# Kernel optimization log

Hardware: AMD Instinct MI355X
Metric: run time of the kernel (lower is better)

The kernel has to match this reference:

```python
import jax, jax.numpy as jnp
import numpy as np

B, T, D, H = 2, 2048, 1024, 16
HS = D // H  # head_size = 64
DFF = 4 * D


def setup_inputs() -> dict:
    key = jax.random.key(0)
    ks = jax.random.split(key, 12)
    s = 0.02
    return {
        "x": jax.random.normal(ks[0], (B, T, D), dtype=jnp.float32),
        "Wq": jax.random.normal(ks[1], (D, D), dtype=jnp.float32) * s,
        "Wk": jax.random.normal(ks[2], (D, D), dtype=jnp.float32) * s,
        "Wv": jax.random.normal(ks[3], (D, D), dtype=jnp.float32) * s,
        "Wo": jax.random.normal(ks[4], (D, D), dtype=jnp.float32) * s,
        "bo": jnp.zeros((D,), dtype=jnp.float32),
        "W1": jax.random.normal(ks[5], (D, DFF), dtype=jnp.float32) * s,
        "b1": jnp.zeros((DFF,), dtype=jnp.float32),
        "W2": jax.random.normal(ks[6], (DFF, D), dtype=jnp.float32) * s,
        "b2": jnp.zeros((D,), dtype=jnp.float32),
        "g1": jnp.ones((D,), dtype=jnp.float32),
        "be1": jnp.zeros((D,), dtype=jnp.float32),
        "g2": jnp.ones((D,), dtype=jnp.float32),
        "be2": jnp.zeros((D,), dtype=jnp.float32),
    }


def layer_norm(x, g, b, eps=1e-5):
    mu = jnp.mean(x, axis=-1, keepdims=True)
    var = jnp.var(x, axis=-1, keepdims=True)
    return (x - mu) * jax.lax.rsqrt(var + eps) * g + b


def attention(x, Wq, Wk, Wv, Wo, bo):
    # x: [B,T,D] -> q,k,v: [B,H,T,HS]
    def split_heads(y):
        return y.reshape(B, T, H, HS).transpose(0, 2, 1, 3)
    q = split_heads(x @ Wq)
    k = split_heads(x @ Wk)
    v = split_heads(x @ Wv)
    scores = jnp.einsum("bhqd,bhkd->bhqk", q, k) / jnp.sqrt(jnp.float32(HS))
    causal = jnp.tril(jnp.ones((T, T), dtype=bool))
    scores = jnp.where(causal, scores, -jnp.inf)
    probs = jax.nn.softmax(scores, axis=-1)
    out = jnp.einsum("bhqk,bhkd->bhqd", probs, v)
    out = out.transpose(0, 2, 1, 3).reshape(B, T, D)
    return out @ Wo + bo


def reference(x, Wq, Wk, Wv, Wo, bo, W1, b1, W2, b2, g1, be1, g2, be2):
    x = x + attention(layer_norm(x, g1, be1), Wq, Wk, Wv, Wo, bo)
    h = layer_norm(x, g2, be2)
    x = x + (jax.nn.relu(h @ W1 + b1) @ W2 + b2)
    return x
```

## Files before the change

### kernel.cpp

```cpp
#include <hip/hip_runtime.h>
#include <stdint.h>

#define Bc   2
#define Tc   2048
#define Dc   1024
#define Hc   16
#define HSc  64
#define DFFc 4096
#define Mc   (Bc * Tc)

using f32x4 = __attribute__((ext_vector_type(4))) float;
using s16x8 = __attribute__((ext_vector_type(8))) short;

__device__ __forceinline__ ushort f2bf(float f) {
  union { float f; uint32_t u; } v; v.f = f;
  uint32_t r = (v.u + 0x7FFFu + ((v.u >> 16) & 1u)) >> 16;
  return (ushort)r;
}
__device__ __forceinline__ float bf2f(ushort u) {
  union { uint32_t u; float f; } v; v.u = ((uint32_t)u) << 16;
  return v.f;
}
__device__ __forceinline__ uint32_t cvtpk(float a, float b) {
  uint32_t r;
  asm volatile("v_cvt_pk_bf16_f32 %0, %1, %2" : "=v"(r) : "v"(a), "v"(b));
  return r;
}
__device__ __forceinline__ float wredsum(float v) {
#pragma unroll
  for (int o = 32; o > 0; o >>= 1) v += __shfl_down(v, o);
  return v;
}

__device__ __forceinline__ void gload16(const ushort* g, ushort* l) {
  __builtin_amdgcn_global_load_lds(
      (const __attribute__((address_space(1))) void*)g,
      (__attribute__((address_space(3))) void*)l, 16, 0, 0);
}

__global__ __launch_bounds__(256) void tcast_all_kernel(
    const float* __restrict__ Wq, const float* __restrict__ Wk,
    const float* __restrict__ Wv, const float* __restrict__ Wo,
    const float* __restrict__ W1, const float* __restrict__ W2,
    ushort* __restrict__ wqkvt, ushort* __restrict__ wot,
    ushort* __restrict__ w1t, ushort* __restrict__ w2t) {
  __shared__ float t[32][33];
  const int id = blockIdx.x;
  const float* src; ushort* dst; int K, N, bx, by;
  if (id < 4096) {
    const int which = id >> 10, local = id & 1023;
    src = (which == 0) ? Wq : (which == 1) ? Wk : (which == 2) ? Wv : Wo;
    dst = (which == 3) ? wot : wqkvt + (size_t)which * 1024 * 1024;
    K = 1024; N = 1024; bx = local & 31; by = local >> 5;
  } else if (id < 8192) {
    const int local = id - 4096;
    src = W1; dst = w1t; K = 1024; N = 4096;
    bx = local & 127; by = local >> 7;
  } else {
    const int local = id - 8192;
    src = W2; dst = w2t; K = 4096; N = 1024;
    bx = local & 31; by = local >> 5;
  }
  const int tid = threadIdx.x;
  const int n0 = bx * 32, k0 = by * 32;
  const int r = tid >> 3, c4 = (tid & 7) * 4;
  const float4 v = *(const float4*)&src[(size_t)(k0 + r) * N + n0 + c4];
  t[r][c4] = v.x; t[r][c4 + 1] = v.y; t[r][c4 + 2] = v.z; t[r][c4 + 3] = v.w;
  __syncthreads();
  ushort4 o;
  o.x = f2bf(t[c4 + 0][r]); o.y = f2bf(t[c4 + 1][r]);
  o.z = f2bf(t[c4 + 2][r]); o.w = f2bf(t[c4 + 3][r]);
  *(ushort4*)&dst[(size_t)(n0 + r) * K + k0 + c4] = o;
}

__global__ __launch_bounds__(256) void ln_kernel(const float* __restrict__ x,
                                                 const float* __restrict__ g,
                                                 const float* __restrict__ b,
                                                 ushort* __restrict__ out) {
  const int row = blockIdx.x;
  const int tid = threadIdx.x;
  const int lane = tid & 63, wave = tid >> 6;
  const float4 v = ((const float4*)(x + (size_t)row * Dc))[tid];
  float s  = v.x + v.y + v.z + v.w;
  float s2 = v.x * v.x + v.y * v.y + v.z * v.z + v.w * v.w;
  __shared__ float rs[4], rs2[4];
  s = wredsum(s); s2 = wredsum(s2);
  if (lane == 0) { rs[wave] = s; rs2[wave] = s2; }
  __syncthreads();
  const float S  = rs[0] + rs[1] + rs[2] + rs[3];
  const float S2 = rs2[0] + rs2[1] + rs2[2] + rs2[3];
  const float mu = S * (1.f / (float)Dc);
  const float rstd = rsqrtf(S2 * (1.f / (float)Dc) - mu * mu + 1e-5f);
  const float4 gv = ((const float4*)g)[tid];
  const float4 bv = ((const float4*)b)[tid];
  ushort4 o;
  o.x = f2bf((v.x - mu) * rstd * gv.x + bv.x);
  o.y = f2bf((v.y - mu) * rstd * gv.y + bv.y);
  o.z = f2bf((v.z - mu) * rstd * gv.z + bv.z);
  o.w = f2bf((v.w - mu) * rstd * gv.w + bv.w);
  ((ushort4*)(out + (size_t)row * Dc))[tid] = o;
}

template <int BM, int NSPLIT, int OUT_BF16, int RELU, int BIAS, int RES, int QKVSPLIT>
__global__ __launch_bounds__(256) void gemm3_kernel(
    const ushort* __restrict__ A, const ushort* __restrict__ Bt,
    const float* __restrict__ bias, const float* __restrict__ res,
    void* __restrict__ C0, void* __restrict__ C1, void* __restrict__ C2,
    int M, int N, int K) {
  constexpr int MF = BM / 32;
  __shared__ __align__(16) ushort As[BM * 64];
  __shared__ __align__(16) ushort Bs[128 * 64];
  const int tid = threadIdx.x;
  const int lane = tid & 63, w = tid >> 6;
  const int wm = w >> 1, wn = w & 1;
  const int row0 = blockIdx.x * BM, col0 = blockIdx.y * 128;
  const int fr = lane & 15, fg = lane >> 4;
  const int kbeg = (NSPLIT > 1) ? blockIdx.z * (K / NSPLIT) : 0;
  const int kend = (NSPLIT > 1) ? kbeg + K / NSPLIT : K;

  f32x4 acc[MF][4] = {};

  for (int k0 = kbeg; k0 < kend; k0 += 64) {
#pragma unroll
    for (int i = 0; i < BM * 8 / 256; i++) {
      const int c = i * 256 + tid;
      const int r = c >> 3, j = c & 7;
      gload16(A + (size_t)(row0 + r) * K + k0 + ((j ^ (r & 7)) << 3),
              As + (i * 256 + w * 64) * 8);
    }
#pragma unroll
    for (int i = 0; i < 4; i++) {
      const int c = i * 256 + tid;
      const int r = c >> 3, j = c & 7;
      gload16(Bt + (size_t)(col0 + r) * K + k0 + ((j ^ (r & 7)) << 3),
              Bs + (i * 256 + w * 64) * 8);
    }
    __syncthreads();

#pragma unroll
    for (int kk = 0; kk < 2; kk++) {
      const int js = ((kk * 4 + fg) ^ (fr & 7)) << 3;
      s16x8 af[MF], bfr[4];
#pragma unroll
      for (int m = 0; m < MF; m++)
        af[m] = *(const s16x8*)&As[(wm * (BM / 2) + m * 16 + fr) * 64 + js];
#pragma unroll
      for (int n = 0; n < 4; n++)
        bfr[n] = *(const s16x8*)&Bs[(wn * 64 + n * 16 + fr) * 64 + js];
#pragma unroll
      for (int m = 0; m < MF; m++)
#pragma unroll
        for (int n = 0; n < 4; n++)
          acc[m][n] = __builtin_amdgcn_mfma_f32_16x16x32_bf16(af[m], bfr[n], acc[m][n], 0, 0, 0);
    }
    __syncthreads();
  }

  if (NSPLIT > 1) {
    float* P = (float*)C0 + (size_t)blockIdx.z * M * N;
#pragma unroll
    for (int m = 0; m < MF; m++)
#pragma unroll
      for (int n = 0; n < 4; n++)
#pragma unroll
        for (int i = 0; i < 4; i++) {
          const int r = row0 + wm * (BM / 2) + m * 16 + fg * 4 + i;
          const int c = col0 + n * 16 + wn * 64 + fr;
          P[(size_t)r * N + c] = acc[m][n][i];
        }
    return;
  }

  void* Cb = C0;
  int cbase = col0;
  if (QKVSPLIT) {
    const int which = col0 >> 10;
    Cb = (which == 0) ? C0 : (which == 1) ? C1 : C2;
    cbase = col0 & 1023;
  }
  const int NW = QKVSPLIT ? 1024 : N;
#pragma unroll
  for (int m = 0; m < MF; m++) {
#pragma unroll
    for (int n = 0; n < 4; n++) {
#pragma unroll
      for (int i = 0; i < 4; i++) {
        const int r = row0 + wm * (BM / 2) + m * 16 + fg * 4 + i;
        const int c = cbase + wn * 64 + n * 16 + fr;
        float v = acc[m][n][i];
        if (BIAS) v += bias[col0 - cbase + c];
        if (RELU) v = fmaxf(v, 0.f);
        if (RES)  v += res[(size_t)r * NW + c];
        if (OUT_BF16) ((ushort*)Cb)[(size_t)r * NW + c] = f2bf(v);
        else          ((float*)Cb)[(size_t)r * NW + c] = v;
      }
    }
  }
}

__global__ __launch_bounds__(256) void sum2_kernel(const float* __restrict__ p0,
                                                   const float* __restrict__ p1,
                                                   const float* __restrict__ bias,
                                                   const float* __restrict__ res,
                                                   float* __restrict__ out) {
  const size_t i = ((size_t)blockIdx.x * 256 + threadIdx.x) * 4;
  const float4 a = *(const float4*)(p0 + i);
  const float4 b = *(const float4*)(p1 + i);
  const float4 r = *(const float4*)(res + i);
  const float4 bs = *(const float4*)(bias + (i & 1023));
  float4 o;
  o.x = a.x + b.x + bs.x + r.x;
  o.y = a.y + b.y + bs.y + r.y;
  o.z = a.z + b.z + bs.z + r.z;
  o.w = a.w + b.w + bs.w + r.w;
  *(float4*)(out + i) = o;
}

__global__ __launch_bounds__(512) void fattn3_kernel(const ushort* __restrict__ Q,
                                                     const ushort* __restrict__ K,
                                                     const ushort* __restrict__ V,
                                                     float* __restrict__ pacc,
                                                     float* __restrict__ pl) {
  __shared__ __align__(16) ushort Kl[2][64][72];
  __shared__ __align__(16) ushort Vt[2][64][72];
  __shared__ __align__(16) uint32_t Pu[8][512];

  const int tid = threadIdx.x;
  const int lane = tid & 63, w = tid >> 6;
  const int fr = lane & 15, fg = lane >> 4;

  const int bh   = blockIdx.x & 31;
  const int rest = blockIdx.x >> 5;
  const int qb   = 15 - (rest >> 1);
  const int z    = rest & 1;
  const int h = bh & 15, b = bh >> 4;
  const int q0 = qb * 128;
  const size_t hbase = (size_t)b * Tc * Dc + (size_t)h * HSc;

  s16x8 qf0, qf1;
  {
    const ushort* qp = Q + hbase + (size_t)(q0 + w * 16 + fr) * Dc + fg * 8;
    qf0 = *(const s16x8*)(qp);
    qf1 = *(const s16x8*)(qp + 32);
  }

  const int kkey = tid >> 3, kd8 = (tid & 7) * 8;
  const int vkey = tid & 63, vd8 = (tid >> 6) * 8;

  const int t0 = z * (qb + 1), t1 = (z + 1) * (qb + 1);
  uint4 kreg = *(const uint4*)(K + hbase + (size_t)(t0 * 64 + kkey) * Dc + kd8);
  uint4 vreg = *(const uint4*)(V + hbase + (size_t)(t0 * 64 + vkey) * Dc + vd8);

  f32x4 acc[4] = {};
  float ps = 0.f;
  const float Cs = 0.18033688f;

  for (int kt = t0; kt < t1; kt++) {
    const int cur = (kt - t0) & 1;
    *(uint4*)&Kl[cur][kkey][kd8] = kreg;
    {
      union { uint4 v; ushort u[8]; } t; t.v = vreg;
#pragma unroll
      for (int j = 0; j < 8; j++) Vt[cur][vd8 + j][vkey] = t.u[j];
    }
    if (kt + 1 < t1) {
      kreg = *(const uint4*)(K + hbase + (size_t)((kt + 1) * 64 + kkey) * Dc + kd8);
      vreg = *(const uint4*)(V + hbase + (size_t)((kt + 1) * 64 + vkey) * Dc + vd8);
    }
    __syncthreads();

    const bool skip = (kt * 64 > q0 + w * 16 + 15);
    if (!skip) {
      f32x4 s[4] = {};
      __builtin_amdgcn_s_setprio(1);
#pragma unroll
      for (int kf = 0; kf < 4; kf++) {
        const s16x8 k0 = *(const s16x8*)&Kl[cur][kf * 16 + fr][fg * 8];
        const s16x8 k1 = *(const s16x8*)&Kl[cur][kf * 16 + fr][32 + fg * 8];
        s[kf] = __builtin_amdgcn_mfma_f32_16x16x32_bf16(k0, qf0, s[kf], 0, 0, 0);
        s[kf] = __builtin_amdgcn_mfma_f32_16x16x32_bf16(k1, qf1, s[kf], 0, 0, 0);
      }
      __builtin_amdgcn_s_setprio(0);

      const bool diag = (kt * 64 + 63 > q0 + w * 16);
      const int qg = q0 + w * 16 + fr;
#pragma unroll
      for (int kf = 0; kf < 4; kf++) {
        float p[4];
#pragma unroll
        for (int i = 0; i < 4; i++) {
          p[i] = exp2f(s[kf][i] * Cs);
          if (diag) {
            const int kg = kt * 64 + kf * 16 + fg * 4 + i;
            if (kg > qg) p[i] = 0.f;
          }
          ps += p[i];
        }
        uint2 pk;
        pk.x = cvtpk(p[0], p[1]);
        pk.y = cvtpk(p[2], p[3]);
        *(uint2*)&Pu[w][(2 * kf + (fg >> 1)) * 64 + fr * 4 + (fg & 1) * 2] = pk;
      }

      const s16x8 pa0 = *(const s16x8*)&Pu[w][fg * 64 + fr * 4];
      const s16x8 pa1 = *(const s16x8*)&Pu[w][(4 + fg) * 64 + fr * 4];
      __builtin_amdgcn_s_setprio(1);
#pragma unroll
      for (int df = 0; df < 4; df++) {
        const s16x8 v0 = *(const s16x8*)&Vt[cur][df * 16 + fr][fg * 8];
        const s16x8 v1 = *(const s16x8*)&Vt[cur][df * 16 + fr][32 + fg * 8];
        acc[df] = __builtin_amdgcn_mfma_f32_16x16x32_bf16(pa0, v0, acc[df], 0, 0, 0);
        acc[df] = __builtin_amdgcn_mfma_f32_16x16x32_bf16(pa1, v1, acc[df], 0, 0, 0);
      }
      __builtin_amdgcn_s_setprio(0);
    }
  }

  ps += __shfl_xor(ps, 16);
  ps += __shfl_xor(ps, 32);
  if (lane < 16)
    pl[(size_t)z * (32 * 2048) + (size_t)bh * 2048 + q0 + w * 16 + lane] = ps;

  float* pa = pacc + (size_t)z * (32ull * 2048 * 64) + (size_t)bh * 2048 * 64;
#pragma unroll
  for (int i = 0; i < 4; i++) {
    const int qr = q0 + w * 16 + fg * 4 + i;
#pragma unroll
    for (int df = 0; df < 4; df++)
      pa[(size_t)qr * 64 + df * 16 + fr] = acc[df][i];
  }
}

__global__ __launch_bounds__(256) void amerge_kernel(const float* __restrict__ pacc,
                                                     const float* __restrict__ pl,
                                                     ushort* __restrict__ O) {
  const int g = blockIdx.x * 256 + threadIdx.x;
  const int d4 = g & 15;
  const int t  = (g >> 4) & 2047;
  const int bh = g >> 15;
  const int h = bh & 15, b = bh >> 4;
  const size_t base = ((size_t)bh * 2048 + t) * 64 + d4 * 4;
  const float4 a = *(const float4*)(pacc + base);
  const float4 c = *(const float4*)(pacc + 32ull * 2048 * 64 + base);
  const float inv = 1.f / (pl[(size_t)bh * 2048 + t] + pl[32 * 2048 + (size_t)bh * 2048 + t]);
  ushort4 o;
  o.x = f2bf((a.x + c.x) * inv);
  o.y = f2bf((a.y + c.y) * inv);
  o.z = f2bf((a.z + c.z) * inv);
  o.w = f2bf((a.w + c.w) * inv);
  *(ushort4*)&O[((size_t)(b * 2048 + t)) * 1024 + h * 64 + d4 * 4] = o;
}

extern "C" void kernel_launch(void* const* d_in, const int* in_sizes, int n_in,
                              void* d_out, int out_size, void* d_ws, size_t ws_size,
                              hipStream_t stream) {
  const float* x   = (const float*)d_in[0];
  const float* Wq  = (const float*)d_in[1];
  const float* Wk  = (const float*)d_in[2];
  const float* Wv  = (const float*)d_in[3];
  const float* Wo  = (const float*)d_in[4];
  const float* bo  = (const float*)d_in[5];
  const float* W1  = (const float*)d_in[6];
  const float* b1  = (const float*)d_in[7];
  const float* W2  = (const float*)d_in[8];
  const float* b2  = (const float*)d_in[9];
  const float* g1  = (const float*)d_in[10];
  const float* be1 = (const float*)d_in[11];
  const float* g2  = (const float*)d_in[12];
  const float* be2 = (const float*)d_in[13];

  char* ws = (char*)d_ws;
  const size_t MB = 1ull << 20;
  ushort* ln1   = (ushort*)(ws + 0 * MB);
  ushort* qb    = (ushort*)(ws + 8 * MB);
  ushort* kb    = (ushort*)(ws + 16 * MB);
  ushort* vb    = (ushort*)(ws + 24 * MB);
  ushort* wqkvt = (ushort*)(ws + 32 * MB);
  ushort* wot   = (ushort*)(ws + 38 * MB);
  ushort* w1t   = (ushort*)(ws + 40 * MB);
  ushort* w2t   = (ushort*)(ws + 48 * MB);
  float*  x1    = (float*)(ws + 56 * MB);
  ushort* hb    = (ushort*)(ws + 72 * MB);
  float*  pacc  = (float*)(ws + 56 * MB);
  float*  plv   = (float*)(ws + 88 * MB);
  float*  fpart = (float*)(ws + 0 * MB);

  tcast_all_kernel<<<12288, 256, 0, stream>>>(Wq, Wk, Wv, Wo, W1, W2,
                                              wqkvt, wot, w1t, w2t);

  ln_kernel<<<Mc, 256, 0, stream>>>(x, g1, be1, ln1);

  gemm3_kernel<128, 1, 1, 0, 0, 0, 1><<<dim3(32, 24), 256, 0, stream>>>(
      ln1, wqkvt, nullptr, nullptr, qb, kb, vb, Mc, 3072, Dc);

  fattn3_kernel<<<1024, 512, 0, stream>>>(qb, kb, vb, pacc, plv);
  amerge_kernel<<<4096, 256, 0, stream>>>(pacc, plv, ln1);

  gemm3_kernel<64, 1, 0, 0, 1, 1, 0><<<dim3(64, 8), 256, 0, stream>>>(
      ln1, wot, bo, x, x1, nullptr, nullptr, Mc, Dc, Dc);

  ln_kernel<<<Mc, 256, 0, stream>>>(x1, g2, be2, qb);

  gemm3_kernel<128, 1, 1, 1, 1, 0, 0><<<dim3(32, 32), 256, 0, stream>>>(
      qb, w1t, b1, nullptr, hb, nullptr, nullptr, Mc, DFFc, Dc);

  gemm3_kernel<64, 2, 0, 0, 0, 0, 0><<<dim3(64, 8, 2), 256, 0, stream>>>(
      hb, w2t, nullptr, nullptr, fpart, nullptr, nullptr, Mc, Dc, DFFc);
  sum2_kernel<<<4096, 256, 0, stream>>>(fpart, fpart + (size_t)Mc * Dc, b2, x1,
                                        (float*)d_out);
}
```

Measured before the change: 222.4 us.

## Add 8-wave GEMM with 256-wide tiles and double-buffered direct-to-LDS loads

Introduces gemm8_kernel, which runs 512 threads per block with larger output tiles (256 columns, 128-256 rows). It double-buffers global-to-LDS loads with explicit vmcnt waits and uses 16x16x32 bf16 MFMA with an XOR-swizzled LDS layout. It replaces gemm3 for the QKV, FFN1 and FFN2 projections to raise data reuse per tile and overlap loads with compute. The trade-off is fewer blocks per GEMM (for example 192 for QKV), which can leave compute units idle, plus higher LDS and register pressure.

```diff
diff --git a/kernel.cpp b/kernel.cpp
--- a/kernel.cpp
+++ b/kernel.cpp
@@ -36,6 +36,12 @@
   __builtin_amdgcn_global_load_lds(
       (const __attribute__((address_space(1))) void*)g,
       (__attribute__((address_space(3))) void*)l, 16, 0, 0);
+}
+
+template <int N> __device__ __forceinline__ void vwait() {
+  if constexpr (N == 0) asm volatile("s_waitcnt vmcnt(0)" ::: "memory");
+  else if constexpr (N == 6) asm volatile("s_waitcnt vmcnt(6)" ::: "memory");
+  else asm volatile("s_waitcnt vmcnt(8)" ::: "memory");
 }
 
 __global__ __launch_bounds__(256) void tcast_all_kernel(
@@ -198,6 +204,148 @@
   }
 }
 
+template <int BM, int NSPLIT, int OUT_BF16, int RELU, int BIAS, int RES, int QKVSPLIT>
+__global__ __launch_bounds__(512, 2) void gemm8_kernel(
+    const ushort* __restrict__ A, const ushort* __restrict__ Bt,
+    const float* __restrict__ bias, const float* __restrict__ res,
+    void* __restrict__ C0, void* __restrict__ C1, void* __restrict__ C2,
+    int M, int N, int K) {
+  constexpr int WR = BM / 2;
+  constexpr int FI = WR / 16;
+  constexpr int QF = FI / 2;
+  constexpr int AIT = BM * 8 / 512;
+  constexpr int LPT = AIT + 4;
+  constexpr int BUFE = (BM + 256) * 64;
+  __shared__ __align__(16) ushort lds[2 * BUFE];
+
+  const int tid = threadIdx.x;
+  const int lane = tid & 63, w = tid >> 6;
+  const int wm = w >> 2, wn = w & 3;
+  const int fr = lane & 15, fg = lane >> 4;
+  const int row0 = blockIdx.x * BM, col0 = blockIdx.y * 256;
+  const int kbeg = (NSPLIT > 1) ? blockIdx.z * (K / NSPLIT) : 0;
+  const int nt = (K / NSPLIT) / 64;
+
+  const int sr = tid >> 3;
+  const int jswz = ((tid & 7) ^ (sr & 7)) << 3;
+
+  f32x4 acc[FI][4] = {};
+
+  auto STAGE = [&](int t, int buf) {
+    const int k0 = kbeg + t * 64;
+    ushort* base = lds + buf * BUFE;
+    const ushort* ga = A + (size_t)(row0 + sr) * K + k0 + jswz;
+#pragma unroll
+    for (int i = 0; i < AIT; ++i)
+      gload16(ga + (size_t)(i * 64) * K, base + (i * 512 + w * 64) * 8);
+    const ushort* gb = Bt + (size_t)(col0 + sr) * K + k0 + jswz;
+#pragma unroll
+    for (int i = 0; i < 4; ++i)
+      gload16(gb + (size_t)(i * 64) * K, base + BM * 64 + (i * 512 + w * 64) * 8);
+  };
+
+  auto COMPUTE = [&](int buf) {
+    const ushort* ab = lds + buf * BUFE;
+    const ushort* bb = ab + BM * 64;
+#pragma unroll
+    for (int q = 0; q < 2; ++q) {
+      s16x8 af[QF][2];
+#pragma unroll
+      for (int fi = 0; fi < QF; ++fi) {
+        const int arow = wm * WR + (q * QF + fi) * 16 + fr;
+#pragma unroll
+        for (int kk = 0; kk < 2; ++kk) {
+          const int ck = (kk * 4 + fg) ^ (arow & 7);
+          af[fi][kk] = *(const s16x8*)&ab[arow * 64 + ck * 8];
+        }
+      }
+#pragma unroll
+      for (int h = 0; h < 2; ++h) {
+        s16x8 bf[2][2];
+#pragma unroll
+        for (int ni = 0; ni < 2; ++ni) {
+          const int brow = wn * 64 + (h * 2 + ni) * 16 + fr;
+#pragma unroll
+          for (int kk = 0; kk < 2; ++kk) {
+            const int ck = (kk * 4 + fg) ^ (brow & 7);
+            bf[ni][kk] = *(const s16x8*)&bb[brow * 64 + ck * 8];
+          }
+        }
+        __builtin_amdgcn_s_setprio(1);
+#pragma unroll
+        for (int fi = 0; fi < QF; ++fi)
+#pragma unroll
+          for (int ni = 0; ni < 2; ++ni)
+#pragma unroll
+            for (int kk = 0; kk < 2; ++kk)
+              acc[q * QF + fi][h * 2 + ni] = __builtin_amdgcn_mfma_f32_16x16x32_bf16(
+                  af[fi][kk], bf[ni][kk], acc[q * QF + fi][h * 2 + ni], 0, 0, 0);
+        __builtin_amdgcn_s_setprio(0);
+      }
+    }
+  };
+
+  STAGE(0, 0);
+  if (nt > 1) STAGE(1, 1);
+  for (int t = 0; t < nt - 1; ++t) {
+    const int cur = t & 1;
+    vwait<LPT>();
+    __builtin_amdgcn_sched_barrier(0);
+    __builtin_amdgcn_s_barrier();
+    __builtin_amdgcn_sched_barrier(0);
+    COMPUTE(cur);
+    __builtin_amdgcn_sched_barrier(0);
+    __builtin_amdgcn_s_barrier();
+    __builtin_amdgcn_sched_barrier(0);
+    if (t + 2 < nt) STAGE(t + 2, cur);
+  }
+  vwait<0>();
+  __builtin_amdgcn_sched_barrier(0);
+  __builtin_amdgcn_s_barrier();
+  __builtin_amdgcn_sched_barrier(0);
+  COMPUTE((nt - 1) & 1);
+
+  if constexpr (NSPLIT > 1) {
+    float* P = (float*)C0 + (size_t)blockIdx.z * M * N;
+#pragma unroll
+    for (int mi = 0; mi < FI; ++mi)
+#pragma unroll
+      for (int ni = 0; ni < 4; ++ni)
+#pragma unroll
+        for (int i = 0; i < 4; ++i) {
+          const int r = row0 + wm * WR + mi * 16 + fg * 4 + i;
+          const int c = col0 + wn * 64 + ni * 16 + fr;
+          P[(size_t)r * N + c] = acc[mi][ni][i];
+        }
+  } else {
+    void* Cb = C0;
+    int cbase = col0;
+    if (QKVSPLIT) {
+      const int which = col0 >> 10;
+      Cb = (which == 0) ? C0 : (which == 1) ? C1 : C2;
+      cbase = col0 & 1023;
+    }
+    const int NW = QKVSPLIT ? 1024 : N;
+#pragma unroll
+    for (int mi = 0; mi < FI; ++mi) {
+#pragma unroll
+      for (int ni = 0; ni < 4; ++ni) {
+#pragma unroll
+        for (int i = 0; i < 4; ++i) {
+          const int r = row0 + wm * WR + mi * 16 + fg * 4 + i;
+          const int c = cbase + wn * 64 + ni * 16 + fr;
+          float v = acc[mi][ni][i];
+          if (BIAS) v += bias[col0 - cbase + c];
+          if (RELU) v = fmaxf(v, 0.f);
+          if (RES)  v += res[(size_t)r * NW + c];
+          if (OUT_BF16) ((ushort*)Cb)[(size_t)r * NW + c] = f2bf(v);
+          else          ((float*)Cb)[(size_t)r * NW + c] = v;
+        }
+      }
+    }
+  }
+}
+
 __global__ __launch_bounds__(256) void sum2_kernel(const float* __restrict__ p0,
                                                    const float* __restrict__ p1,
                                                    const float* __restrict__ bias,
@@ -390,7 +538,7 @@
 
   ln_kernel<<<Mc, 256, 0, stream>>>(x, g1, be1, ln1);
 
-  gemm3_kernel<128, 1, 1, 0, 0, 0, 1><<<dim3(32, 24), 256, 0, stream>>>(
+  gemm8_kernel<256, 1, 1, 0, 0, 0, 1><<<dim3(16, 12), 512, 0, stream>>>(
       ln1, wqkvt, nullptr, nullptr, qb, kb, vb, Mc, 3072, Dc);
 
   fattn3_kernel<<<1024, 512, 0, stream>>>(qb, kb, vb, pacc, plv);
@@ -401,10 +549,10 @@
 
   ln_kernel<<<Mc, 256, 0, stream>>>(x1, g2, be2, qb);
 
-  gemm3_kernel<128, 1, 1, 1, 1, 0, 0><<<dim3(32, 32), 256, 0, stream>>>(
+  gemm8_kernel<256, 1, 1, 1, 1, 0, 0><<<dim3(16, 16), 512, 0, stream>>>(
       qb, w1t, b1, nullptr, hb, nullptr, nullptr, Mc, DFFc, Dc);
 
-  gemm3_kernel<64, 2, 0, 0, 0, 0, 0><<<dim3(64, 8, 2), 256, 0, stream>>>(
+  gemm8_kernel<128, 2, 0, 0, 0, 0, 0><<<dim3(32, 4, 2), 512, 0, stream>>>(
       hb, w2t, nullptr, nullptr, fpart, nullptr, nullptr, Mc, Dc, DFFc);
   sum2_kernel<<<4096, 256, 0, stream>>>(fpart, fpart + (size_t)Mc * Dc, b2, x1,
                                         (float*)d_out);
```

Result: faster. 216.6 us (-2.6%).
